# Performance work log

Measured on AMD Instinct MI355X. Metric: run time of the kernel, lower is better.

## Reference

```python
import jax, jax.numpy as jnp
import numpy as np

A = 256       # number of nodes (node_vec.shape[0])
F = 256       # dim_feature
C = 32        # dim_outerproduct
EPS = 1e-5    # NORM_SMALL


def setup_inputs() -> dict:
    key = jax.random.key(0)
    ks = jax.random.split(key, 8)
    inp = {
        "node_vec": jax.random.normal(ks[0], (A, F), dtype=jnp.float32),
        "node_mask": jnp.ones((A,), dtype=jnp.float32),
        "ln_scale": jnp.ones((F,), dtype=jnp.float32),
        "ln_bias": jnp.zeros((F,), dtype=jnp.float32),
        "Wl": jax.random.normal(ks[1], (F, C), dtype=jnp.float32) / np.sqrt(F),
        "bl": jnp.zeros((C,), dtype=jnp.float32),
        "Wr": jax.random.normal(ks[2], (F, C), dtype=jnp.float32) / np.sqrt(F),
        "br": jnp.zeros((C,), dtype=jnp.float32),
        "Wo": jax.random.normal(ks[3], (C * C, F), dtype=jnp.float32) / np.sqrt(C * C),
        "bo": jnp.zeros((F,), dtype=jnp.float32),
    }
    return inp


def reference(node_vec, node_mask, ln_scale, ln_bias, Wl, bl, Wr, br, Wo, bo):
    # LayerNorm over the feature axis
    mu = jnp.mean(node_vec, axis=-1, keepdims=True)
    var = jnp.mean(jnp.square(node_vec - mu), axis=-1, keepdims=True)
    act = (node_vec - mu) * jax.lax.rsqrt(var + EPS) * ln_scale + ln_bias

    # Dual projections, masked per node
    left_act = (act @ Wl + bl) * node_mask[:, None]    # [A, C]
    right_act = (act @ Wr + br) * node_mask[:, None]   # [A, C]

    # Explicit outer product. Original computes a [C*A, A*C] matmul then
    # reshapes/transposes to [A, A, C*C]; equivalently:
    # out4[a, b, c, d] = left_act[a, c] * right_act[b, d]
    out_act = jnp.einsum('ac,bd->abcd', left_act, right_act)  # [A, A, C, C]
    out_act = out_act.reshape((node_vec.shape[0], node_vec.shape[0], C * C))

    # Output projection
    return out_act @ Wo + bo  # [A, A, F]
```

## Files before the change

kernel.cpp:

```cpp
#include <hip/hip_runtime.h>
#include <hip/hip_bf16.h>

#define A_N 256
#define F_N 256
#define C_N 32

__global__ __launch_bounds__(256) void ln_proj_kernel(
    const float* __restrict__ node_vec, const float* __restrict__ node_mask,
    const float* __restrict__ ln_scale, const float* __restrict__ ln_bias,
    const float* __restrict__ Wl, const float* __restrict__ bl,
    const float* __restrict__ Wr, const float* __restrict__ br,
    float* __restrict__ left, float* __restrict__ right) {
  const int a = blockIdx.x;
  const int t = threadIdx.x;
  __shared__ float sAct[F_N];
  __shared__ float sRed[8];
  __shared__ float sPl[8][C_N];
  __shared__ float sPr[8][C_N];

  float x = node_vec[a * F_N + t];

  float s = x;
  for (int off = 32; off; off >>= 1) s += __shfl_down(s, off, 64);
  const int wave = t >> 6, lane = t & 63;
  if (lane == 0) sRed[wave] = s;
  __syncthreads();
  if (t == 0) sRed[4] = (sRed[0] + sRed[1] + sRed[2] + sRed[3]) * (1.0f / F_N);
  __syncthreads();
  const float mu = sRed[4];
  const float d = x - mu;

  s = d * d;
  for (int off = 32; off; off >>= 1) s += __shfl_down(s, off, 64);
  if (lane == 0) sRed[wave] = s;
  __syncthreads();
  if (t == 0) {
    float v = (sRed[0] + sRed[1] + sRed[2] + sRed[3]) * (1.0f / F_N);
    sRed[5] = rsqrtf(v + 1e-5f);
  }
  __syncthreads();
  const float act = d * sRed[5] * ln_scale[t] + ln_bias[t];
  sAct[t] = act;
  __syncthreads();

  const int c = t & 31, seg = t >> 5;
  float pl = 0.f, pr = 0.f;
  const float* actp = &sAct[seg * 32];
#pragma unroll
  for (int j = 0; j < 32; ++j) {
    const float av = actp[j];
    const int widx = (seg * 32 + j) * C_N + c;
    pl = fmaf(av, Wl[widx], pl);
    pr = fmaf(av, Wr[widx], pr);
  }
  sPl[seg][c] = pl;
  sPr[seg][c] = pr;
  __syncthreads();
  if (t < C_N) {
    const float m = node_mask[a];
    float suml = bl[t], sumr = br[t];
#pragma unroll
    for (int sg = 0; sg < 8; ++sg) { suml += sPl[sg][t]; sumr += sPr[sg][t]; }
    left[a * C_N + t] = suml * m;
    right[a * C_N + t] = sumr * m;
  }
}

__global__ __launch_bounds__(256) void compT_kernel(
    const float* __restrict__ right, const float* __restrict__ Wo,
    float* __restrict__ T) {
  const int c = blockIdx.y;
  const int b0 = blockIdx.x * 16;
  const int f = threadIdx.x;
  __shared__ float sWo[C_N * F_N];
  __shared__ float sR[16 * C_N];

#pragma unroll
  for (int d = 0; d < C_N; ++d)
    sWo[d * F_N + f] = Wo[(c * C_N + d) * F_N + f];
  sR[f] = right[b0 * C_N + f];
  sR[256 + f] = right[b0 * C_N + 256 + f];
  __syncthreads();

#pragma unroll 4
  for (int b = 0; b < 16; ++b) {
    float acc = 0.f;
#pragma unroll
    for (int d = 0; d < C_N; ++d)
      acc = fmaf(sR[b * C_N + d], sWo[d * F_N + f], acc);
    T[c * (A_N * F_N) + (b0 + b) * F_N + f] = acc;
  }
}

__global__ __launch_bounds__(256) void out_kernel(
    const float* __restrict__ left, const float* __restrict__ T,
    const float* __restrict__ bo, float* __restrict__ out) {
  const int b = blockIdx.y;
  const int a0 = blockIdx.x * 64;
  const int f = threadIdx.x;
  __shared__ float sT[C_N * F_N];
  __shared__ float sL[64 * C_N];

#pragma unroll
  for (int c = 0; c < C_N; ++c)
    sT[c * F_N + f] = T[c * (A_N * F_N) + b * F_N + f];
#pragma unroll
  for (int k = 0; k < 8; ++k) {
    const int idx = k * 256 + f;
    sL[idx] = left[a0 * C_N + idx];
  }
  const float biasf = bo[f];
  __syncthreads();

  for (int a = 0; a < 64; a += 4) {
    float acc0 = biasf, acc1 = biasf, acc2 = biasf, acc3 = biasf;
#pragma unroll
    for (int c = 0; c < C_N; ++c) {
      const float tv = sT[c * F_N + f];
      acc0 = fmaf(sL[(a + 0) * C_N + c], tv, acc0);
      acc1 = fmaf(sL[(a + 1) * C_N + c], tv, acc1);
      acc2 = fmaf(sL[(a + 2) * C_N + c], tv, acc2);
      acc3 = fmaf(sL[(a + 3) * C_N + c], tv, acc3);
    }
    const int base = (a0 + a) * (A_N * F_N) + b * F_N + f;
    out[base] = acc0;
    out[base + 1 * A_N * F_N] = acc1;
    out[base + 2 * A_N * F_N] = acc2;
    out[base + 3 * A_N * F_N] = acc3;
  }
}

extern "C" void kernel_launch(void* const* d_in, const int* in_sizes, int n_in,
                              void* d_out, int out_size, void* d_ws, size_t ws_size,
                              hipStream_t stream) {
  const float* node_vec  = (const float*)d_in[0];
  const float* node_mask = (const float*)d_in[1];
  const float* ln_scale  = (const float*)d_in[2];
  const float* ln_bias   = (const float*)d_in[3];
  const float* Wl        = (const float*)d_in[4];
  const float* bl        = (const float*)d_in[5];
  const float* Wr        = (const float*)d_in[6];
  const float* br        = (const float*)d_in[7];
  const float* Wo        = (const float*)d_in[8];
  const float* bo        = (const float*)d_in[9];
  float* out = (float*)d_out;

  float* left  = (float*)d_ws;
  float* right = left + A_N * C_N;
  float* T     = right + A_N * C_N;

  ln_proj_kernel<<<A_N, 256, 0, stream>>>(node_vec, node_mask, ln_scale, ln_bias,
                                          Wl, bl, Wr, br, left, right);
  compT_kernel<<<dim3(16, 32), 256, 0, stream>>>(right, Wo, T);
  out_kernel<<<dim3(4, A_N), 256, 0, stream>>>(left, T, bo, out);
}
```

Measured before the change: 127.5 us.

## Register-tile compT and out kernels, relayout T as [b][c][f], vectorize

```diff
diff --git a/kernel.cpp b/kernel.cpp
--- a/kernel.cpp
+++ b/kernel.cpp
@@ -1,5 +1,4 @@
 #include <hip/hip_runtime.h>
-#include <hip/hip_bf16.h>
 
 #define A_N 256
 #define F_N 256
@@ -82,14 +81,21 @@
   sR[256 + f] = right[b0 * C_N + 256 + f];
   __syncthreads();
 
-#pragma unroll 4
-  for (int b = 0; b < 16; ++b) {
-    float acc = 0.f;
+  float acc[16];
 #pragma unroll
-    for (int d = 0; d < C_N; ++d)
-      acc = fmaf(sR[b * C_N + d], sWo[d * F_N + f], acc);
-    T[c * (A_N * F_N) + (b0 + b) * F_N + f] = acc;
+  for (int b = 0; b < 16; ++b) acc[b] = 0.f;
+
+#pragma unroll
+  for (int d = 0; d < C_N; ++d) {
+    const float wv = sWo[d * F_N + f];
+#pragma unroll
+    for (int b = 0; b < 16; ++b)
+      acc[b] = fmaf(sR[b * C_N + d], wv, acc[b]);
   }
+
+#pragma unroll
+  for (int b = 0; b < 16; ++b)
+    T[(size_t)(b0 + b) * (C_N * F_N) + c * F_N + f] = acc[b];
 }
 
 __global__ __launch_bounds__(256) void out_kernel(
@@ -97,37 +103,47 @@
     const float* __restrict__ bo, float* __restrict__ out) {
   const int b = blockIdx.y;
   const int a0 = blockIdx.x * 64;
-  const int f = threadIdx.x;
+  const int t = threadIdx.x;
+  const int fq = t & 63;
+  const int arow = t >> 6;
+
   __shared__ float sT[C_N * F_N];
   __shared__ float sL[64 * C_N];
 
+  float4* sT4 = (float4*)sT;
+  const float4* Tg4 = (const float4*)(T + (size_t)b * (C_N * F_N));
 #pragma unroll
-  for (int c = 0; c < C_N; ++c)
-    sT[c * F_N + f] = T[c * (A_N * F_N) + b * F_N + f];
+  for (int k = 0; k < 8; ++k) sT4[k * 256 + t] = Tg4[k * 256 + t];
+  float4* sL4 = (float4*)sL;
+  const float4* Lg4 = (const float4*)(left + a0 * C_N);
 #pragma unroll
-  for (int k = 0; k < 8; ++k) {
-    const int idx = k * 256 + f;
-    sL[idx] = left[a0 * C_N + idx];
-  }
-  const float biasf = bo[f];
+  for (int k = 0; k < 2; ++k) sL4[k * 256 + t] = Lg4[k * 256 + t];
+  const float4 bias4 = ((const float4*)bo)[fq];
   __syncthreads();
 
-  for (int a = 0; a < 64; a += 4) {
-    float acc0 = biasf, acc1 = biasf, acc2 = biasf, acc3 = biasf;
+  float4 acc[16];
 #pragma unroll
-    for (int c = 0; c < C_N; ++c) {
-      const float tv = sT[c * F_N + f];
-      acc0 = fmaf(sL[(a + 0) * C_N + c], tv, acc0);
-      acc1 = fmaf(sL[(a + 1) * C_N + c], tv, acc1);
-      acc2 = fmaf(sL[(a + 2) * C_N + c], tv, acc2);
-      acc3 = fmaf(sL[(a + 3) * C_N + c], tv, acc3);
+  for (int i = 0; i < 16; ++i) acc[i] = bias4;
+
+  const float* sLrow = &sL[(arow * 16) * C_N];
+#pragma unroll 8
+  for (int c = 0; c < C_N; ++c) {
+    const float4 tv = sT4[c * 64 + fq];
+#pragma unroll
+    for (int i = 0; i < 16; ++i) {
+      const float lv = sLrow[i * C_N + c];
+      acc[i].x = fmaf(lv, tv.x, acc[i].x);
+      acc[i].y = fmaf(lv, tv.y, acc[i].y);
+      acc[i].z = fmaf(lv, tv.z, acc[i].z);
+      acc[i].w = fmaf(lv, tv.w, acc[i].w);
     }
-    const int base = (a0 + a) * (A_N * F_N) + b * F_N + f;
-    out[base] = acc0;
-    out[base + 1 * A_N * F_N] = acc1;
-    out[base + 2 * A_N * F_N] = acc2;
-    out[base + 3 * A_N * F_N] = acc3;
   }
+
+  float4* out4 = (float4*)out;
+  const size_t rowq = (size_t)(A_N * F_N) / 4;
+#pragma unroll
+  for (int i = 0; i < 16; ++i)
+    out4[(size_t)(a0 + arow * 16 + i) * rowq + (size_t)b * 64 + fq] = acc[i];
 }
 
 extern "C" void kernel_launch(void* const* d_in, const int* in_sizes, int n_in,
```

Measured after the change: 114.7 us. 10.0% less time.
